# Optimization experiments

Hardware: AMD Instinct MI355X
Metric: run time of the kernel (lower is better)

Reference implementation:

```python
import jax, jax.numpy as jnp
import numpy as np

N, NFEAT, NHID, NCLASS = 8192, 512, 256, 2
ALPHA = 0.5


def setup_inputs() -> dict:
    key = jax.random.key(0)
    k1, k2, k3, k4, k5 = jax.random.split(key, 5)
    x = jax.random.normal(k1, (N, NFEAT), dtype=jnp.float32)
    adj = jax.random.uniform(k2, (N, N), dtype=jnp.float32)
    # GraphConvolution init: uniform(-stdv, stdv), stdv = 1/sqrt(out_features)
    s1 = 1.0 / np.sqrt(NHID)
    W1 = jax.random.uniform(k3, (NFEAT, NHID), dtype=jnp.float32, minval=-s1, maxval=s1)
    s2 = 1.0 / np.sqrt(NCLASS)
    W2 = jax.random.uniform(k4, (NHID, NCLASS), dtype=jnp.float32, minval=-s2, maxval=s2)
    b2 = jax.random.uniform(k5, (NCLASS,), dtype=jnp.float32, minval=-s2, maxval=s2)
    return {"x": x, "adj": adj, "W1": W1, "W2": W2, "b2": b2}


def _mid_filter_2(adj, alpha):
    # D_row = diag(rowsum^-0.5), D_col = diag(colsum^-0.5); inf -> 0
    d_row = jnp.power(jnp.sum(adj, axis=1), -0.5)
    d_row = jnp.where(jnp.isinf(d_row), 0.0, d_row)
    d_col = jnp.power(jnp.sum(adj, axis=0), -0.5)
    d_col = jnp.where(jnp.isinf(d_col), 0.0, d_col)
    # (adj @ D_col)^T @ D_row)^T == d_row[:,None] * adj * d_col[None,:]
    DAD = d_row[:, None] * adj * d_col[None, :]
    I = jnp.eye(adj.shape[0], dtype=adj.dtype)
    return jnp.matmul(alpha * I - DAD, I + DAD)


def reference(x, adj, W1, W2, b2):
    adj_f = _mid_filter_2(adj, ALPHA)
    # hidden layer (no bias): relu(adj_f @ (x @ W1)); dropout = identity (eval)
    h = jax.nn.relu(jnp.matmul(adj_f, jnp.matmul(x, W1)))
    # output layer (with bias)
    out = jnp.matmul(adj_f, jnp.matmul(h, W2)) + b2
    return jax.nn.log_softmax(out, axis=-1)
```

## Files before the change

### kernel.cpp

```cpp
#include <hip/hip_runtime.h>
#include <hip/hip_bf16.h>

typedef unsigned short u16;
typedef unsigned int u32;
typedef __attribute__((ext_vector_type(8))) short short8;
typedef __attribute__((ext_vector_type(4))) float f32x4;

#define NN 8192
#define NF 512
#define NH 256
#define SPLITZ 4

__device__ __forceinline__ float bf2f(u32 u) {
  union { u32 i; float f; } v; v.i = u << 16; return v.f;
}
__device__ __forceinline__ u16 f2bf(float f) {
  union { __hip_bfloat16 b; u16 u; } v; v.b = __float2bfloat16(f); return v.u;
}
__device__ __forceinline__ u32 pack2(float a, float b) {
  return (u32)f2bf(a) | ((u32)f2bf(b) << 16);
}

__global__ __launch_bounds__(256) void conv_adj_k(const float* __restrict__ adj,
                                                  u16* __restrict__ adjb,
                                                  float* __restrict__ rowsum,
                                                  float* __restrict__ colsum) {
  __shared__ float red[4][128];
  const int t = threadIdx.x;
  const int w = t >> 6, lane = t & 63;
  const int c0 = blockIdx.x * 2048 + t * 8;
  const int r0 = blockIdx.y * 128;
  float cp[8] = {0.f, 0.f, 0.f, 0.f, 0.f, 0.f, 0.f, 0.f};
  for (int r = 0; r < 128; ++r) {
    const size_t base = (size_t)(r0 + r) * NN + c0;
    float4 v0 = *(const float4*)(adj + base);
    float4 v1 = *(const float4*)(adj + base + 4);
    uint4 pk;
    pk.x = pack2(v0.x, v0.y); pk.y = pack2(v0.z, v0.w);
    pk.z = pack2(v1.x, v1.y); pk.w = pack2(v1.z, v1.w);
    *(uint4*)(adjb + base) = pk;
    cp[0] += v0.x; cp[1] += v0.y; cp[2] += v0.z; cp[3] += v0.w;
    cp[4] += v1.x; cp[5] += v1.y; cp[6] += v1.z; cp[7] += v1.w;
    float rs = (v0.x + v0.y) + (v0.z + v0.w) + ((v1.x + v1.y) + (v1.z + v1.w));
#pragma unroll
    for (int off = 32; off > 0; off >>= 1) rs += __shfl_down(rs, off, 64);
    if (lane == 0) red[w][r] = rs;
  }
  __syncthreads();
  if (t < 128)
    atomicAdd(&rowsum[r0 + t], red[0][t] + red[1][t] + red[2][t] + red[3][t]);
#pragma unroll
  for (int j = 0; j < 8; ++j) atomicAdd(&colsum[c0 + j], cp[j]);
}

__global__ void finalize_k(const float* __restrict__ sums, float* __restrict__ d, int n) {
  const int i = blockIdx.x * blockDim.x + threadIdx.x;
  if (i < n) {
    const float s = sums[i];
    d[i] = (s > 0.f) ? rsqrtf(s) : 0.f;
  }
}

__global__ __launch_bounds__(256) void convx_k(const float* __restrict__ x,
                                               u16* __restrict__ xb) {
  const size_t i = ((size_t)blockIdx.x * 256 + threadIdx.x) * 8;
  float4 v0 = *(const float4*)(x + i);
  float4 v1 = *(const float4*)(x + i + 4);
  uint4 pk;
  pk.x = pack2(v0.x, v0.y); pk.y = pack2(v0.z, v0.w);
  pk.z = pack2(v1.x, v1.y); pk.w = pack2(v1.z, v1.w);
  *(uint4*)(xb + i) = pk;
}

__global__ __launch_bounds__(256) void convw1_k(const float* __restrict__ in,
                                                u16* __restrict__ out) {
  __shared__ float tile[32][33];
  const int tx = threadIdx.x & 31, ty = threadIdx.x >> 5;
  const int c0 = blockIdx.x * 32;
  const int r0 = blockIdx.y * 32;
#pragma unroll
  for (int d = 0; d < 32; d += 8)
    tile[ty + d][tx] = in[(size_t)(r0 + ty + d) * NH + c0 + tx];
  __syncthreads();
#pragma unroll
  for (int d = 0; d < 32; d += 8)
    out[(size_t)(c0 + ty + d) * NF + r0 + tx] = f2bf(tile[tx][ty + d]);
}

__device__ __forceinline__ void stage128(const u16* __restrict__ A, int lda,
                                         const u16* __restrict__ Bt, int ldb,
                                         int m0, int n0, int kk,
                                         u16* as_, u16* bs_, int tid) {
#pragma unroll
  for (int h = 0; h < 2; ++h) {
    const int slot = tid + h * 256;
    const int row = slot >> 2, kc = slot & 3;
    const u16* srcA = A + (size_t)(m0 + row) * lda + kk + kc * 8;
    __builtin_amdgcn_global_load_lds((const __attribute__((address_space(1))) void*)srcA,
                                     (__attribute__((address_space(3))) void*)(as_ + slot * 8),
                                     16, 0, 0);
    const u16* srcB = Bt + (size_t)(n0 + row) * ldb + kk + kc * 8;
    __builtin_amdgcn_global_load_lds((const __attribute__((address_space(1))) void*)srcB,
                                     (__attribute__((address_space(3))) void*)(bs_ + slot * 8),
                                     16, 0, 0);
  }
}

__global__ __launch_bounds__(256) void gemm_k(const u16* __restrict__ A, int lda,
                                              const u16* __restrict__ Bt, int ldb,
                                              int kChunk, float* __restrict__ out) {
  __shared__ __align__(16) u16 As[2][128 * 32];
  __shared__ __align__(16) u16 Bs[2][128 * 32];
  const int tid = threadIdx.x;
  const int w = tid >> 6, lane = tid & 63;
  const int lq = lane >> 4, lr = lane & 15;
  const int wr = (w >> 1) * 64, wc = (w & 1) * 64;
  const int m0 = blockIdx.x * 128;
  const int n0 = blockIdx.y * 128;
  const int kk0 = blockIdx.z * kChunk;
  const int nk = kChunk >> 5;

  f32x4 acc[4][4] = {};

  stage128(A, lda, Bt, ldb, m0, n0, kk0, As[0], Bs[0], tid);
  for (int kt = 0; kt < nk; ++kt) {
    const int cur = kt & 1;
    __syncthreads();
    if (kt + 1 < nk)
      stage128(A, lda, Bt, ldb, m0, n0, kk0 + ((kt + 1) << 5), As[cur ^ 1], Bs[cur ^ 1], tid);
    short8 a[4], b[4];
#pragma unroll
    for (int i = 0; i < 4; ++i)
      a[i] = *(const short8*)(As[cur] + (wr + i * 16 + lr) * 32 + lq * 8);
#pragma unroll
    for (int i = 0; i < 4; ++i)
      b[i] = *(const short8*)(Bs[cur] + (wc + i * 16 + lr) * 32 + lq * 8);
#pragma unroll
    for (int i = 0; i < 4; ++i)
#pragma unroll
      for (int j = 0; j < 4; ++j)
        acc[i][j] = __builtin_amdgcn_mfma_f32_16x16x32_bf16(a[i], b[j], acc[i][j], 0, 0, 0);
  }

  float* o = out + (size_t)blockIdx.z * ((size_t)NN * NH);
#pragma unroll
  for (int i = 0; i < 4; ++i)
#pragma unroll
    for (int j = 0; j < 4; ++j) {
      const int gn = n0 + wc + j * 16 + lr;
      const int gm0 = m0 + wr + i * 16 + lq * 4;
#pragma unroll
      for (int r = 0; r < 4; ++r)
        o[(size_t)(gm0 + r) * NH + gn] = acc[i][j][r];
    }
}

__global__ __launch_bounds__(256) void t1_k(const float* __restrict__ P,
                                            const float* __restrict__ dcol,
                                            u16* __restrict__ B1t) {
  __shared__ float tile[32][33];
  const int tx = threadIdx.x & 31, ty = threadIdx.x >> 5;
  const int c0 = blockIdx.x * 32;
  const int r0 = blockIdx.y * 32;
#pragma unroll
  for (int d = 0; d < 32; d += 8) {
    const int rr = r0 + ty + d;
    tile[ty + d][tx] = dcol[rr] * P[(size_t)rr * NH + c0 + tx];
  }
  __syncthreads();
#pragma unroll
  for (int d = 0; d < 32; d += 8)
    B1t[(size_t)(c0 + ty + d) * NN + r0 + tx] = f2bf(tile[tx][ty + d]);
}

__global__ __launch_bounds__(256) void r2_k(const float* __restrict__ Qp,
                                            const float* __restrict__ drow,
                                            const float* __restrict__ dcol,
                                            float* __restrict__ Q1,
                                            u16* __restrict__ B2t) {
  __shared__ float tile[32][33];
  const int tx = threadIdx.x & 31, ty = threadIdx.x >> 5;
  const int c0 = blockIdx.x * 32;
  const int r0 = blockIdx.y * 32;
  const size_t sl = (size_t)NN * NH;
#pragma unroll
  for (int d = 0; d < 32; d += 8) {
    const int rr = r0 + ty + d;
    const size_t idx = (size_t)rr * NH + c0 + tx;
    const float s = (Qp[idx] + Qp[idx + sl]) + (Qp[idx + 2 * sl] + Qp[idx + 3 * sl]);
    const float q = drow[rr] * s;
    Q1[idx] = q;
    tile[ty + d][tx] = dcol[rr] * q;
  }
  __syncthreads();
#pragma unroll
  for (int d = 0; d < 32; d += 8)
    B2t[(size_t)(c0 + ty + d) * NN + r0 + tx] = f2bf(tile[tx][ty + d]);
}

__global__ __launch_bounds__(256) void r3_k(const float* __restrict__ Hp,
                                            const float* __restrict__ P,
                                            const float* __restrict__ Q1,
                                            const float* __restrict__ drow,
                                            u16* __restrict__ Hb) {
  const size_t i = ((size_t)blockIdx.x * 256 + threadIdx.x) * 4;
  const int row = (int)(i >> 8);
  const size_t sl = (size_t)NN * NH;
  float4 a = *(const float4*)(Hp + i);
  float4 b = *(const float4*)(Hp + i + sl);
  float4 c = *(const float4*)(Hp + i + 2 * sl);
  float4 d = *(const float4*)(Hp + i + 3 * sl);
  float4 p = *(const float4*)(P + i);
  float4 q = *(const float4*)(Q1 + i);
  const float dr = drow[row];
  const float h0 = fmaxf(0.5f * p.x - 0.5f * q.x - dr * ((a.x + b.x) + (c.x + d.x)), 0.f);
  const float h1 = fmaxf(0.5f * p.y - 0.5f * q.y - dr * ((a.y + b.y) + (c.y + d.y)), 0.f);
  const float h2 = fmaxf(0.5f * p.z - 0.5f * q.z - dr * ((a.z + b.z) + (c.z + d.z)), 0.f);
  const float h3 = fmaxf(0.5f * p.w - 0.5f * q.w - dr * ((a.w + b.w) + (c.w + d.w)), 0.f);
  uint2 pk;
  pk.x = pack2(h0, h1);
  pk.y = pack2(h2, h3);
  *(uint2*)(Hb + i) = pk;
}

__global__ __launch_bounds__(256) void r_k(const u16* __restrict__ H,
                                           const float* __restrict__ W2,
                                           const float* __restrict__ dcol,
                                           float* __restrict__ R, float* __restrict__ B3) {
  const int w = threadIdx.x >> 6, lane = threadIdx.x & 63;
  const int i = blockIdx.x * 4 + w;
  uint2 hv = *(const uint2*)(H + (size_t)i * NH + lane * 4);
  float4 w01 = *(const float4*)(W2 + lane * 8);
  float4 w23 = *(const float4*)(W2 + lane * 8 + 4);
  const float h0 = bf2f(hv.x & 0xffffu), h1 = bf2f(hv.x >> 16);
  const float h2 = bf2f(hv.y & 0xffffu), h3 = bf2f(hv.y >> 16);
  float a0 = h0 * w01.x + h1 * w01.z + h2 * w23.x + h3 * w23.z;
  float a1 = h0 * w01.y + h1 * w01.w + h2 * w23.y + h3 * w23.w;
#pragma unroll
  for (int off = 32; off > 0; off >>= 1) {
    a0 += __shfl_down(a0, off, 64);
    a1 += __shfl_down(a1, off, 64);
  }
  if (lane == 0) {
    R[i * 2] = a0;
    R[i * 2 + 1] = a1;
    const float dc = dcol[i];
    B3[i * 2] = dc * a0;
    B3[i * 2 + 1] = dc * a1;
  }
}

__global__ __launch_bounds__(256) void gemv_k(
    const u16* __restrict__ adjb, const float* __restrict__ B,
    const float* __restrict__ drow, const float* __restrict__ dcol,
    const float* __restrict__ Rin, const float* __restrict__ S1in,
    const float* __restrict__ b2, float* __restrict__ S1out,
    float* __restrict__ B4, float* __restrict__ outp, int mode) {
  const int i = blockIdx.x;
  const int t = threadIdx.x;
  float a0 = 0.f, a1 = 0.f;
#pragma unroll
  for (int c = 0; c < 4; ++c) {
    const int col = c * 2048 + t * 8;
    uint4 av = *(const uint4*)(adjb + (size_t)i * NN + col);
    const u32* aw = (const u32*)&av;
    float bv[16];
    *(float4*)(bv) = *(const float4*)(B + col * 2);
    *(float4*)(bv + 4) = *(const float4*)(B + col * 2 + 4);
    *(float4*)(bv + 8) = *(const float4*)(B + col * 2 + 8);
    *(float4*)(bv + 12) = *(const float4*)(B + col * 2 + 12);
#pragma unroll
    for (int j = 0; j < 8; ++j) {
      const u32 a = aw[j >> 1];
      const float aval = bf2f((j & 1) ? (a >> 16) : (a & 0xffffu));
      a0 += aval * bv[2 * j];
      a1 += aval * bv[2 * j + 1];
    }
  }
#pragma unroll
  for (int off = 32; off > 0; off >>= 1) {
    a0 += __shfl_down(a0, off, 64);
    a1 += __shfl_down(a1, off, 64);
  }
  __shared__ float red[8];
  const int w = t >> 6, lane = t & 63;
  if (lane == 0) { red[w] = a0; red[4 + w] = a1; }
  __syncthreads();
  if (t == 0) {
    float s0 = (red[0] + red[1]) + (red[2] + red[3]);
    float s1 = (red[4] + red[5]) + (red[6] + red[7]);
    const float dr = drow[i];
    s0 *= dr; s1 *= dr;
    if (mode == 0) {
      S1out[i * 2] = s0;
      S1out[i * 2 + 1] = s1;
      const float dc = dcol[i];
      B4[i * 2] = dc * s0;
      B4[i * 2 + 1] = dc * s1;
    } else {
      const float l0 = 0.5f * Rin[i * 2] - 0.5f * S1in[i * 2] - s0 + b2[0];
      const float l1 = 0.5f * Rin[i * 2 + 1] - 0.5f * S1in[i * 2 + 1] - s1 + b2[1];
      const float m = fmaxf(l0, l1);
      const float lse = m + logf(__expf(l0 - m) + __expf(l1 - m));
      outp[i * 2] = l0 - lse;
      outp[i * 2 + 1] = l1 - lse;
    }
  }
}

extern "C" void kernel_launch(void* const* d_in, const int* in_sizes, int n_in,
                              void* d_out, int out_size, void* d_ws, size_t ws_size,
                              hipStream_t stream) {
  (void)in_sizes; (void)n_in; (void)out_size; (void)ws_size;
  const float* x   = (const float*)d_in[0];
  const float* adj = (const float*)d_in[1];
  const float* W1  = (const float*)d_in[2];
  const float* W2  = (const float*)d_in[3];
  const float* b2  = (const float*)d_in[4];
  float* outp = (float*)d_out;

  char* ws = (char*)d_ws;
  size_t off = 0;
  auto alloc = [&](size_t bytes) -> char* {
    char* p = ws + off;
    off += (bytes + 255) & ~(size_t)255;
    return p;
  };
  u16* adjb  = (u16*)alloc((size_t)NN * NN * 2);
  u16* xb    = (u16*)alloc((size_t)NN * NF * 2);
  u16* W1t   = (u16*)alloc((size_t)NH * NF * 2);
  float* rowsum = (float*)alloc((size_t)NN * 4);
  float* colsum = (float*)alloc((size_t)NN * 4);
  float* drow   = (float*)alloc((size_t)NN * 4);
  float* dcol   = (float*)alloc((size_t)NN * 4);
  float* P   = (float*)alloc((size_t)NN * NH * 4);
  u16* B1t   = (u16*)alloc((size_t)NH * NN * 2);
  float* Qp  = (float*)alloc((size_t)SPLITZ * NN * NH * 4);
  float* Q1  = (float*)alloc((size_t)NN * NH * 4);
  u16* B2t   = (u16*)alloc((size_t)NH * NN * 2);
  u16* Hb    = (u16*)alloc((size_t)NN * NH * 2);
  float* R   = (float*)alloc((size_t)NN * 2 * 4);
  float* B3  = (float*)alloc((size_t)NN * 2 * 4);
  float* S1  = (float*)alloc((size_t)NN * 2 * 4);
  float* B4  = (float*)alloc((size_t)NN * 2 * 4);
  float* Hp  = Qp;

  (void)hipMemsetAsync(rowsum, 0, (size_t)2 * NN * 4, stream);

  conv_adj_k<<<dim3(4, 64), 256, 0, stream>>>(adj, adjb, rowsum, colsum);
  finalize_k<<<64, 256, 0, stream>>>(rowsum, drow, 2 * NN);
  convx_k<<<2048, 256, 0, stream>>>(x, xb);
  convw1_k<<<dim3(8, 16), 256, 0, stream>>>(W1, W1t);

  gemm_k<<<dim3(64, 2, 1), 256, 0, stream>>>(xb, NF, W1t, NF, NF, P);
  t1_k<<<dim3(8, 256), 256, 0, stream>>>(P, dcol, B1t);

  gemm_k<<<dim3(64, 2, SPLITZ), 256, 0, stream>>>(adjb, NN, B1t, NN, NN / SPLITZ, Qp);
  r2_k<<<dim3(8, 256), 256, 0, stream>>>(Qp, drow, dcol, Q1, B2t);

  gemm_k<<<dim3(64, 2, SPLITZ), 256, 0, stream>>>(adjb, NN, B2t, NN, NN / SPLITZ, Hp);
  r3_k<<<2048, 256, 0, stream>>>(Hp, P, Q1, drow, Hb);

  r_k<<<NN / 4, 256, 0, stream>>>(Hb, W2, dcol, R, B3);
  gemv_k<<<NN, 256, 0, stream>>>(adjb, B3, drow, dcol, nullptr, nullptr, nullptr, S1, B4, nullptr, 0);
  gemv_k<<<NN, 256, 0, stream>>>(adjb, B4, drow, dcol, R, S1, b2, nullptr, nullptr, outp, 1);
}
```

Baseline: 674.4 us.

## Replace atomic row/col sums with partial buffers and swap GEMM grid order

The adjacency conversion kernel now uses 1024 blocks of 32 rows instead of 256 blocks of 128 rows. It writes per-block partial row and column sums to scratch buffers instead of doing atomicAdds. A new reduction kernel folds the partials and computes the rsqrt scalings, which removes the memset and the finalize kernel. The GEMM grid is also transposed so that the two N-tiles sharing an A row-panel run next to each other, which should improve L2 reuse of the large adjacency panel. The cost is extra scratch traffic (an 8 MB column-partial buffer) and a serial 256-way column reduction per thread.

Result: no change. 664.1 us (-1.5%).

```diff
diff --git a/kernel.cpp b/kernel.cpp
--- a/kernel.cpp
+++ b/kernel.cpp
@@ -10,6 +10,7 @@
 #define NF 512
 #define NH 256
 #define SPLITZ 4
+#define RB 256
 
 __device__ __forceinline__ float bf2f(u32 u) {
   union { u32 i; float f; } v; v.i = u << 16; return v.f;
@@ -23,15 +24,16 @@
 
 __global__ __launch_bounds__(256) void conv_adj_k(const float* __restrict__ adj,
                                                   u16* __restrict__ adjb,
-                                                  float* __restrict__ rowsum,
-                                                  float* __restrict__ colsum) {
-  __shared__ float red[4][128];
+                                                  float* __restrict__ rowsum_part,
+                                                  float* __restrict__ colsum_part) {
+  __shared__ float red[4][32];
   const int t = threadIdx.x;
   const int w = t >> 6, lane = t & 63;
-  const int c0 = blockIdx.x * 2048 + t * 8;
-  const int r0 = blockIdx.y * 128;
+  const int s = blockIdx.x;
+  const int c0 = s * 2048 + t * 8;
+  const int r0 = blockIdx.y * 32;
   float cp[8] = {0.f, 0.f, 0.f, 0.f, 0.f, 0.f, 0.f, 0.f};
-  for (int r = 0; r < 128; ++r) {
+  for (int r = 0; r < 32; ++r) {
     const size_t base = (size_t)(r0 + r) * NN + c0;
     float4 v0 = *(const float4*)(adj + base);
     float4 v1 = *(const float4*)(adj + base + 4);
@@ -47,18 +49,25 @@
     if (lane == 0) red[w][r] = rs;
   }
   __syncthreads();
-  if (t < 128)
-    atomicAdd(&rowsum[r0 + t], red[0][t] + red[1][t] + red[2][t] + red[3][t]);
-#pragma unroll
-  for (int j = 0; j < 8; ++j) atomicAdd(&colsum[c0 + j], cp[j]);
-}
-
-__global__ void finalize_k(const float* __restrict__ sums, float* __restrict__ d, int n) {
-  const int i = blockIdx.x * blockDim.x + threadIdx.x;
-  if (i < n) {
-    const float s = sums[i];
-    d[i] = (s > 0.f) ? rsqrtf(s) : 0.f;
-  }
+  if (t < 32)
+    rowsum_part[(size_t)s * NN + r0 + t] =
+        (red[0][t] + red[1][t]) + (red[2][t] + red[3][t]);
+  float* cdst = colsum_part + (size_t)blockIdx.y * NN + c0;
+  *(float4*)cdst = make_float4(cp[0], cp[1], cp[2], cp[3]);
+  *(float4*)(cdst + 4) = make_float4(cp[4], cp[5], cp[6], cp[7]);
+}
+
+__global__ __launch_bounds__(256) void reduce_sums_k(const float* __restrict__ rowp,
+                                                     const float* __restrict__ colp,
+                                                     float* __restrict__ drow,
+                                                     float* __restrict__ dcol) {
+  const int i = blockIdx.x * 256 + threadIdx.x;
+  const float rs = (rowp[i] + rowp[NN + i]) + (rowp[2 * NN + i] + rowp[3 * NN + i]);
+  drow[i] = (rs > 0.f) ? rsqrtf(rs) : 0.f;
+  float cs = 0.f;
+#pragma unroll 8
+  for (int rb = 0; rb < RB; ++rb) cs += colp[(size_t)rb * NN + i];
+  dcol[i] = (cs > 0.f) ? rsqrtf(cs) : 0.f;
 }
 
 __global__ __launch_bounds__(256) void convx_k(const float* __restrict__ x,
@@ -115,8 +124,8 @@
   const int w = tid >> 6, lane = tid & 63;
   const int lq = lane >> 4, lr = lane & 15;
   const int wr = (w >> 1) * 64, wc = (w & 1) * 64;
-  const int m0 = blockIdx.x * 128;
-  const int n0 = blockIdx.y * 128;
+  const int n0 = blockIdx.x * 128;
+  const int m0 = blockIdx.y * 128;
   const int kk0 = blockIdx.z * kChunk;
   const int nk = kChunk >> 5;
 
@@ -329,10 +338,10 @@
   u16* adjb  = (u16*)alloc((size_t)NN * NN * 2);
   u16* xb    = (u16*)alloc((size_t)NN * NF * 2);
   u16* W1t   = (u16*)alloc((size_t)NH * NF * 2);
-  float* rowsum = (float*)alloc((size_t)NN * 4);
-  float* colsum = (float*)alloc((size_t)NN * 4);
-  float* drow   = (float*)alloc((size_t)NN * 4);
-  float* dcol   = (float*)alloc((size_t)NN * 4);
+  float* rowp = (float*)alloc((size_t)4 * NN * 4);
+  float* colp = (float*)alloc((size_t)RB * NN * 4);
+  float* drow = (float*)alloc((size_t)NN * 4);
+  float* dcol = (float*)alloc((size_t)NN * 4);
   float* P   = (float*)alloc((size_t)NN * NH * 4);
   u16* B1t   = (u16*)alloc((size_t)NH * NN * 2);
   float* Qp  = (float*)alloc((size_t)SPLITZ * NN * NH * 4);
@@ -345,20 +354,18 @@
   float* B4  = (float*)alloc((size_t)NN * 2 * 4);
   float* Hp  = Qp;
 
-  (void)hipMemsetAsync(rowsum, 0, (size_t)2 * NN * 4, stream);
-
-  conv_adj_k<<<dim3(4, 64), 256, 0, stream>>>(adj, adjb, rowsum, colsum);
-  finalize_k<<<64, 256, 0, stream>>>(rowsum, drow, 2 * NN);
+  conv_adj_k<<<dim3(4, RB), 256, 0, stream>>>(adj, adjb, rowp, colp);
+  reduce_sums_k<<<NN / 256, 256, 0, stream>>>(rowp, colp, drow, dcol);
   convx_k<<<2048, 256, 0, stream>>>(x, xb);
   convw1_k<<<dim3(8, 16), 256, 0, stream>>>(W1, W1t);
 
-  gemm_k<<<dim3(64, 2, 1), 256, 0, stream>>>(xb, NF, W1t, NF, NF, P);
+  gemm_k<<<dim3(2, 64, 1), 256, 0, stream>>>(xb, NF, W1t, NF, NF, P);
   t1_k<<<dim3(8, 256), 256, 0, stream>>>(P, dcol, B1t);
 
-  gemm_k<<<dim3(64, 2, SPLITZ), 256, 0, stream>>>(adjb, NN, B1t, NN, NN / SPLITZ, Qp);
+  gemm_k<<<dim3(2, 64, SPLITZ), 256, 0, stream>>>(adjb, NN, B1t, NN, NN / SPLITZ, Qp);
   r2_k<<<dim3(8, 256), 256, 0, stream>>>(Qp, drow, dcol, Q1, B2t);
 
-  gemm_k<<<dim3(64, 2, SPLITZ), 256, 0, stream>>>(adjb, NN, B2t, NN, NN / SPLITZ, Hp);
+  gemm_k<<<dim3(2, 64, SPLITZ), 256, 0, stream>>>(adjb, NN, B2t, NN, NN / SPLITZ, Hp);
   r3_k<<<2048, 256, 0, stream>>>(Hp, P, Q1, drow, Hb);
 
   r_k<<<NN / 4, 256, 0, stream>>>(Hb, W2, dcol, R, B3);
```
